# Kernel optimization log

Measured on AMD Instinct MI355X. Metric: run time of the kernel, lower is better.

Reference implementation:

```python
import jax, jax.numpy as jnp
import numpy as np

B, N, T, E = 8, 512, 2048, 4096
D, TD, L = 768, 128, 4
V, TYPES = 30522, 64
MAX_NODE_LEN = 512


def setup_inputs() -> dict:
    key = jax.random.key(0)
    ks = jax.random.split(key, 12)
    tok_per_node = T // N  # 4 tokens per node
    node_types = jax.random.randint(ks[0], (B, N), 0, TYPES)
    node_token_ids = jax.random.randint(ks[1], (B, T), 0, V)
    token_seg_ids = jnp.tile(jnp.arange(T, dtype=jnp.int32) // tok_per_node, (B, 1))
    node_token_lens = jnp.full((B, N), tok_per_node, dtype=jnp.int32)
    graph_node_lens = jnp.full((B,), N, dtype=jnp.int32)
    edge_src = jax.random.randint(ks[2], (B, E), 0, N)
    edge_dst = jax.random.randint(ks[3], (B, E), 0, N)
    # edges_attrs used as PyG edge_weight (original passes LongTensor); cast to float
    edge_weight = jax.random.randint(ks[4], (B, E), 1, 4).astype(jnp.float32)
    s = 0.02
    type_table = jax.random.normal(ks[5], (TYPES, TD)) * s
    word_emb = jax.random.normal(ks[6], (V, D)) * s
    fusion_w = jax.random.normal(ks[7], (TD + D, D)) * s
    fusion_b = jnp.zeros((D,), jnp.float32)
    ggnn_w = jax.random.normal(ks[8], (L, D, D)) * s  # per-layer message weight
    gru_w_ih = jax.random.normal(ks[9], (3 * D, D)) * s  # [W_ir; W_iz; W_in]
    gru_w_hh = jax.random.normal(ks[10], (3 * D, D)) * s
    gru_b_ih = jnp.zeros((3 * D,), jnp.float32)
    gru_b_hh = jnp.zeros((3 * D,), jnp.float32)
    return dict(node_types=node_types, node_token_ids=node_token_ids,
                token_seg_ids=token_seg_ids, node_token_lens=node_token_lens,
                graph_node_lens=graph_node_lens, edge_src=edge_src,
                edge_dst=edge_dst, edge_weight=edge_weight,
                type_table=type_table, word_emb=word_emb,
                fusion_w=fusion_w, fusion_b=fusion_b, ggnn_w=ggnn_w,
                gru_w_ih=gru_w_ih, gru_w_hh=gru_w_hh,
                gru_b_ih=gru_b_ih, gru_b_hh=gru_b_hh)


def reference(node_types, node_token_ids, token_seg_ids, node_token_lens,
              graph_node_lens, edge_src, edge_dst, edge_weight,
              type_table, word_emb, fusion_w, fusion_b, ggnn_w,
              gru_w_ih, gru_w_hh, gru_b_ih, gru_b_hh):
    # --- embed lookups ---
    type_e = type_table[node_types]          # [B, N, TD]
    tok_e = word_emb[node_token_ids]         # [B, T, D]
    # --- ragged per-node token segment-mean ---
    seg_sum = jax.vmap(lambda d, s: jax.ops.segment_sum(d, s, num_segments=N))(
        tok_e, token_seg_ids)                # [B, N, D]
    text_e = seg_sum / node_token_lens[..., None].astype(seg_sum.dtype)
    # --- embed fusion ---
    fused = jnp.concatenate([type_e, text_e], axis=-1)  # [B, N, TD+D]
    h = jnp.einsum('bnf,fd->bnd', fused, fusion_w) + fusion_b  # [B, N, D]

    # --- GatedGraphConv: L rounds of (linear -> weighted scatter-add -> GRU) ---
    def scatter(m, src, dst, w):
        return jnp.zeros((N, m.shape[-1]), m.dtype).at[dst].add(m[src] * w[:, None])

    for l in range(L):
        m = jnp.einsum('bnd,de->bne', h, ggnn_w[l])
        agg = jax.vmap(scatter)(m, edge_src, edge_dst, edge_weight)  # [B, N, D]
        gi = agg @ gru_w_ih.T + gru_b_ih
        gh = h @ gru_w_hh.T + gru_b_hh
        ir, iz, in_ = jnp.split(gi, 3, axis=-1)
        hr, hz, hn = jnp.split(gh, 3, axis=-1)
        r = jax.nn.sigmoid(ir + hr)
        z = jax.nn.sigmoid(iz + hz)
        n = jnp.tanh(in_ + r * hn)
        h = (1.0 - z) * n + z * h

    # --- copy first min(node_lens, max_node_len) rows into zero-initialized res ---
    W = min(N, MAX_NODE_LEN)
    keep = jnp.minimum(graph_node_lens, MAX_NODE_LEN)           # [B]
    valid = jnp.arange(W)[None, :] < keep[:, None]              # [B, W]
    return jnp.where(valid[..., None], h[:, :W], 0.0)           # [B, W, D]
```

## Files before the change

kernel.cpp:

```cpp
#include <hip/hip_runtime.h>
#include <hip/hip_bf16.h>
#include <math.h>

namespace {
constexpr int B_  = 8;
constexpr int N_  = 512;
constexpr int T_  = 2048;
constexpr int E_  = 4096;
constexpr int D_  = 768;
constexpr int TD_ = 128;
constexpr int L_  = 4;
constexpr int F_  = TD_ + D_;
constexpr int G3_ = 3 * D_;
constexpr int BN  = B_ * N_;
constexpr int W_  = 512;
constexpr int TPN = T_ / N_;
}

typedef short bf16x8 __attribute__((ext_vector_type(8)));
typedef float f32x4  __attribute__((ext_vector_type(4)));

typedef const __attribute__((address_space(1))) void* gas1_cvp;
typedef __attribute__((address_space(3))) void*       as3_vp;

__device__ __forceinline__ unsigned short f2b(float f) {
    union { float f; unsigned u; } v; v.f = f;
    unsigned r = v.u + 0x7FFFu + ((v.u >> 16) & 1u);
    return (unsigned short)(r >> 16);
}
__device__ __forceinline__ float b2f(unsigned short u) {
    union { unsigned u; float f; } v; v.u = ((unsigned)u) << 16;
    return v.f;
}


__global__ void embed_fuse_kernel(const int* __restrict__ node_types,
                                  const int* __restrict__ tok_ids,
                                  const int* __restrict__ lens,
                                  const float* __restrict__ type_table,
                                  const float* __restrict__ word_emb,
                                  unsigned short* __restrict__ fused_bf)
{
    int i = blockIdx.x * blockDim.x + threadIdx.x;
    if (i >= BN * (F_ / 4)) return;
    int c4 = i % (F_ / 4);
    int bn = i / (F_ / 4);
    if (c4 < TD_ / 4) {
        int ty = node_types[bn];
        float4 v = *(const float4*)&type_table[(long long)ty * TD_ + c4 * 4];
        *(ushort4*)&fused_bf[(long long)bn * F_ + c4 * 4] =
            make_ushort4(f2b(v.x), f2b(v.y), f2b(v.z), f2b(v.w));
    } else {
        int d4 = c4 - TD_ / 4;
        int b  = bn / N_;
        int nn = bn % N_;
        float inv = 1.0f / (float)lens[bn];
        const int* tp = &tok_ids[b * T_ + nn * TPN];
        float sx = 0.f, sy = 0.f, sz = 0.f, sw = 0.f;
#pragma unroll
        for (int j = 0; j < TPN; ++j) {
            int tok = tp[j];
            float4 e = *(const float4*)&word_emb[(long long)tok * D_ + d4 * 4];
            sx += e.x; sy += e.y; sz += e.z; sw += e.w;
        }
        *(ushort4*)&fused_bf[(long long)bn * F_ + TD_ + d4 * 4] =
            make_ushort4(f2b(sx * inv), f2b(sy * inv), f2b(sz * inv), f2b(sw * inv));
    }
}

__global__ void adj_build_kernel(const int* __restrict__ esrc,
                                 const int* __restrict__ edst,
                                 const float* __restrict__ ew,
                                 float* __restrict__ adj)
{
    int i = blockIdx.x * blockDim.x + threadIdx.x;
    if (i >= B_ * E_) return;
    int b = i / E_;
    int s = esrc[i];
    int d = edst[i];
    atomicAdd(&adj[((long long)b * N_ + d) * N_ + s], ew[i]);
}


__global__ void cvt_f32_bf16(const float* __restrict__ s, unsigned short* __restrict__ d, int n4)
{
    int i = blockIdx.x * blockDim.x + threadIdx.x;
    if (i >= n4) return;
    float4 v = ((const float4*)s)[i];
    ((ushort4*)d)[i] = make_ushort4(f2b(v.x), f2b(v.y), f2b(v.z), f2b(v.w));
}

__global__ void transpose_cvt(const float* __restrict__ s, unsigned short* __restrict__ d,
                              int R, int C)
{
    __shared__ float t[32][33];
    long long lo = (long long)blockIdx.z * R * C;
    s += lo; d += lo;
    int c0 = blockIdx.x * 32, r0 = blockIdx.y * 32;
    int tx = threadIdx.x, ty = threadIdx.y;
#pragma unroll
    for (int j = 0; j < 4; ++j)
        t[ty + j * 8][tx] = s[(long long)(r0 + ty + j * 8) * C + c0 + tx];
    __syncthreads();
#pragma unroll
    for (int j = 0; j < 4; ++j)
        d[(long long)(c0 + ty + j * 8) * R + r0 + tx] = f2b(t[tx][ty + j * 8]);
}


template <int MODE>
__global__ __launch_bounds__(256)
void gemm_mfma(const unsigned short* __restrict__ Ag,
               const unsigned short* __restrict__ Bg,
               void* __restrict__ Cg, void* __restrict__ C2g,
               const float* __restrict__ bias,
               int M, int N, int K, long long sA, long long sB, long long sC)
{
    __shared__ __align__(16) short As[128 * 32];
    __shared__ __align__(16) short Bs[128 * 32];

    const int tid  = threadIdx.x;
    const int lane = tid & 63;
    const int wv   = tid >> 6;
    const int wr   = wv >> 1, wc = wv & 1;
    const int row0 = blockIdx.y * 128;
    const int col0 = blockIdx.x * 128;

    const unsigned short* A  = Ag + blockIdx.z * sA;
    const unsigned short* Bm = Bg + blockIdx.z * sB;

    f32x4 acc[4][4] = {};

    const int srow = lane >> 2;
    const int sk   = (lane & 3) * 8;

    const int fr = lane & 15;
    const int kc = (lane >> 4) * 8;

    for (int k0 = 0; k0 < K; k0 += 32) {
#pragma unroll
        for (int r = 0; r < 2; ++r) {
            const unsigned short* ga = A  + (long long)(row0 + r * 64 + wv * 16 + srow) * K + k0 + sk;
            __builtin_amdgcn_global_load_lds((gas1_cvp)ga,
                (as3_vp)(As + (r * 64 + wv * 16) * 32), 16, 0, 0);
            const unsigned short* gb = Bm + (long long)(col0 + r * 64 + wv * 16 + srow) * K + k0 + sk;
            __builtin_amdgcn_global_load_lds((gas1_cvp)gb,
                (as3_vp)(Bs + (r * 64 + wv * 16) * 32), 16, 0, 0);
        }
        __syncthreads();

        bf16x8 fa[4], fb[4];
#pragma unroll
        for (int m = 0; m < 4; ++m)
            fa[m] = *(const bf16x8*)&As[(wr * 64 + m * 16 + fr) * 32 + kc];
#pragma unroll
        for (int n = 0; n < 4; ++n)
            fb[n] = *(const bf16x8*)&Bs[(wc * 64 + n * 16 + fr) * 32 + kc];
#pragma unroll
        for (int m = 0; m < 4; ++m)
#pragma unroll
            for (int n = 0; n < 4; ++n)
                acc[m][n] = __builtin_amdgcn_mfma_f32_16x16x32_bf16(fa[m], fb[n], acc[m][n], 0, 0, 0);
        __syncthreads();
    }

    const int fq = lane >> 4;
#pragma unroll
    for (int m = 0; m < 4; ++m) {
        const int gr = row0 + wr * 64 + m * 16 + fq * 4;
#pragma unroll
        for (int n = 0; n < 4; ++n) {
            const int gc = col0 + wc * 64 + n * 16 + fr;
            float v0 = acc[m][n][0], v1 = acc[m][n][1], v2 = acc[m][n][2], v3 = acc[m][n][3];
            if (bias != nullptr) {
                float bv = bias[gc];
                v0 += bv; v1 += bv; v2 += bv; v3 += bv;
            }
            if constexpr (MODE == 0 || MODE == 1) {
                float* C = (float*)Cg + blockIdx.z * sC;
                C[(long long)(gr + 0) * N + gc] = v0;
                C[(long long)(gr + 1) * N + gc] = v1;
                C[(long long)(gr + 2) * N + gc] = v2;
                C[(long long)(gr + 3) * N + gc] = v3;
                if constexpr (MODE == 1) {
                    unsigned short* C2 = (unsigned short*)C2g;
                    C2[(long long)(gr + 0) * N + gc] = f2b(v0);
                    C2[(long long)(gr + 1) * N + gc] = f2b(v1);
                    C2[(long long)(gr + 2) * N + gc] = f2b(v2);
                    C2[(long long)(gr + 3) * N + gc] = f2b(v3);
                }
            } else if constexpr (MODE == 2) {
                unsigned short* C = (unsigned short*)Cg + blockIdx.z * sC;
                C[(long long)(gr + 0) * N + gc] = f2b(v0);
                C[(long long)(gr + 1) * N + gc] = f2b(v1);
                C[(long long)(gr + 2) * N + gc] = f2b(v2);
                C[(long long)(gr + 3) * N + gc] = f2b(v3);
            } else {
                unsigned short* C = (unsigned short*)Cg;
                int b = gr >> 9;
                int s = gr & 511;
                ushort4 pk = make_ushort4(f2b(v0), f2b(v1), f2b(v2), f2b(v3));
                *(ushort4*)&C[((long long)b * N + gc) * 512 + s] = pk;
            }
        }
    }
}


__global__ void gru_kernel(const unsigned short* __restrict__ gi,
                           const unsigned short* __restrict__ gh,
                           const float* __restrict__ bih, const float* __restrict__ bhh,
                           float* __restrict__ h, unsigned short* __restrict__ hb)
{
    int i = blockIdx.x * blockDim.x + threadIdx.x;
    if (i >= BN * (D_ / 4)) return;
    int d4 = i % (D_ / 4);
    int rn = i / (D_ / 4);
    int d = d4 * 4;
    const unsigned short* gir = gi + (long long)rn * G3_;
    const unsigned short* ghr = gh + (long long)rn * G3_;
    ushort4 uir = *(const ushort4*)&gir[d];
    ushort4 uiz = *(const ushort4*)&gir[D_ + d];
    ushort4 uin = *(const ushort4*)&gir[2 * D_ + d];
    ushort4 uhr = *(const ushort4*)&ghr[d];
    ushort4 uhz = *(const ushort4*)&ghr[D_ + d];
    ushort4 uhn = *(const ushort4*)&ghr[2 * D_ + d];
    float4 hv = *(const float4*)&h[(long long)rn * D_ + d];

    float a_ir[4] = {b2f(uir.x), b2f(uir.y), b2f(uir.z), b2f(uir.w)};
    float a_iz[4] = {b2f(uiz.x), b2f(uiz.y), b2f(uiz.z), b2f(uiz.w)};
    float a_in[4] = {b2f(uin.x), b2f(uin.y), b2f(uin.z), b2f(uin.w)};
    float a_hr[4] = {b2f(uhr.x), b2f(uhr.y), b2f(uhr.z), b2f(uhr.w)};
    float a_hz[4] = {b2f(uhz.x), b2f(uhz.y), b2f(uhz.z), b2f(uhz.w)};
    float a_hn[4] = {b2f(uhn.x), b2f(uhn.y), b2f(uhn.z), b2f(uhn.w)};
    float a_h[4]  = {hv.x, hv.y, hv.z, hv.w};
    float outv[4];
#pragma unroll
    for (int u = 0; u < 4; ++u) {
        float r = 1.f / (1.f + expf(-(a_ir[u] + bih[d + u] + a_hr[u] + bhh[d + u])));
        float z = 1.f / (1.f + expf(-(a_iz[u] + bih[D_ + d + u] + a_hz[u] + bhh[D_ + d + u])));
        float n = tanhf(a_in[u] + bih[2 * D_ + d + u] + r * (a_hn[u] + bhh[2 * D_ + d + u]));
        outv[u] = (1.f - z) * n + z * a_h[u];
    }
    float4 o; o.x = outv[0]; o.y = outv[1]; o.z = outv[2]; o.w = outv[3];
    *(float4*)&h[(long long)rn * D_ + d] = o;
    *(ushort4*)&hb[(long long)rn * D_ + d] = make_ushort4(f2b(outv[0]), f2b(outv[1]),
                                                          f2b(outv[2]), f2b(outv[3]));
}


__global__ void out_mask_kernel(const int* __restrict__ gl, float* __restrict__ h)
{
    int i = blockIdx.x * blockDim.x + threadIdx.x;
    if (i >= B_ * W_ * (D_ / 4)) return;
    int d4 = i % (D_ / 4);
    int bw = i / (D_ / 4);
    int b = bw / W_;
    int w = bw % W_;
    int keep = min(gl[b], W_);
    if (w >= keep)
        *(float4*)&h[((long long)b * W_ + w) * D_ + d4 * 4] = make_float4(0.f, 0.f, 0.f, 0.f);
}


extern "C" void kernel_launch(void* const* d_in, const int* in_sizes, int n_in,
                              void* d_out, int out_size, void* d_ws, size_t ws_size,
                              hipStream_t stream)
{
    (void)in_sizes; (void)n_in; (void)out_size; (void)ws_size;

    const int*   node_types      = (const int*)d_in[0];
    const int*   node_token_ids  = (const int*)d_in[1];
    const int*   node_token_lens = (const int*)d_in[3];
    const int*   graph_node_lens = (const int*)d_in[4];
    const int*   edge_src        = (const int*)d_in[5];
    const int*   edge_dst        = (const int*)d_in[6];
    const float* edge_weight     = (const float*)d_in[7];
    const float* type_table      = (const float*)d_in[8];
    const float* word_emb        = (const float*)d_in[9];
    const float* fusion_w        = (const float*)d_in[10];
    const float* fusion_b        = (const float*)d_in[11];
    const float* ggnn_w          = (const float*)d_in[12];
    const float* gru_w_ih        = (const float*)d_in[13];
    const float* gru_w_hh        = (const float*)d_in[14];
    const float* gru_b_ih        = (const float*)d_in[15];
    const float* gru_b_hh        = (const float*)d_in[16];

    float* h = (float*)d_out;

    char* p = (char*)d_ws;
    auto carve = [&](size_t bytes) { char* r = p; p += (bytes + 255) & ~(size_t)255; return r; };

    unsigned short* gi_bf   = (unsigned short*)carve((size_t)BN * G3_ * 2);
    unsigned short* gh_bf   = (unsigned short*)carve((size_t)BN * G3_ * 2);
    unsigned short* h_bf    = (unsigned short*)carve((size_t)BN * D_ * 2);
    unsigned short* fused_bf= (unsigned short*)carve((size_t)BN * F_ * 2);
    float*          adj     = (float*)carve((size_t)B_ * N_ * N_ * 4);
    unsigned short* adj_bf  = (unsigned short*)carve((size_t)B_ * N_ * N_ * 2);
    unsigned short* mT      = (unsigned short*)carve((size_t)B_ * D_ * N_ * 2);
    unsigned short* agg_bf  = (unsigned short*)carve((size_t)BN * D_ * 2);
    unsigned short* fwT     = (unsigned short*)carve((size_t)D_ * F_ * 2);
    unsigned short* gwT     = (unsigned short*)carve((size_t)L_ * D_ * D_ * 2);
    unsigned short* wih_bf  = (unsigned short*)carve((size_t)G3_ * D_ * 2);
    unsigned short* whh_bf  = (unsigned short*)carve((size_t)G3_ * D_ * 2);

    hipMemsetAsync(adj, 0, (size_t)B_ * N_ * N_ * 4, stream);

    {   int n = BN * (F_ / 4);
        embed_fuse_kernel<<<(n + 255) / 256, 256, 0, stream>>>(
            node_types, node_token_ids, node_token_lens, type_table, word_emb, fused_bf); }
    {   int n = B_ * E_;
        adj_build_kernel<<<(n + 255) / 256, 256, 0, stream>>>(edge_src, edge_dst, edge_weight, adj); }

    cvt_f32_bf16<<<(B_ * N_ * N_ / 4 + 255) / 256, 256, 0, stream>>>(adj, adj_bf, B_ * N_ * N_ / 4);
    cvt_f32_bf16<<<(G3_ * D_ / 4 + 255) / 256, 256, 0, stream>>>(gru_w_ih, wih_bf, G3_ * D_ / 4);
    cvt_f32_bf16<<<(G3_ * D_ / 4 + 255) / 256, 256, 0, stream>>>(gru_w_hh, whh_bf, G3_ * D_ / 4);
    transpose_cvt<<<dim3(D_ / 32, F_ / 32, 1), dim3(32, 8), 0, stream>>>(fusion_w, fwT, F_, D_);
    transpose_cvt<<<dim3(D_ / 32, D_ / 32, L_), dim3(32, 8), 0, stream>>>(ggnn_w, gwT, D_, D_);

    dim3 blk(256);
    gemm_mfma<1><<<dim3(D_ / 128, BN / 128, 1), blk, 0, stream>>>(
        fused_bf, fwT, h, h_bf, fusion_b, BN, D_, F_, 0, 0, 0);

    for (int l = 0; l < L_; ++l) {
        gemm_mfma<3><<<dim3(D_ / 128, BN / 128, 1), blk, 0, stream>>>(
            h_bf, gwT + (size_t)l * D_ * D_, mT, nullptr, nullptr, BN, D_, D_, 0, 0, 0);
        gemm_mfma<2><<<dim3(D_ / 128, N_ / 128, B_), blk, 0, stream>>>(
            adj_bf, mT, agg_bf, nullptr, nullptr, N_, D_, N_,
            (long long)N_ * N_, (long long)D_ * N_, (long long)N_ * D_);
        gemm_mfma<2><<<dim3(G3_ / 128, BN / 128, 1), blk, 0, stream>>>(
            agg_bf, wih_bf, gi_bf, nullptr, nullptr, BN, G3_, D_, 0, 0, 0);
        gemm_mfma<2><<<dim3(G3_ / 128, BN / 128, 1), blk, 0, stream>>>(
            h_bf, whh_bf, gh_bf, nullptr, nullptr, BN, G3_, D_, 0, 0, 0);
        int n = BN * (D_ / 4);
        gru_kernel<<<(n + 255) / 256, 256, 0, stream>>>(gi_bf, gh_bf, gru_b_ih, gru_b_hh, h, h_bf);
    }

    {   int n = B_ * W_ * (D_ / 4);
        out_mask_kernel<<<(n + 255) / 256, 256, 0, stream>>>(graph_node_lens, h); }
}
```

Measured before the change: 723.9 us.

## Double-buffer GEMM LDS, merge GRU GEMMs, fuse mask and weight conversions

The GEMM main loop now uses two LDS buffers so the next K-tile's global-to-LDS load is issued before computing on the current one, aiming to hide load latency. The two GRU input and hidden GEMMs are merged into one launch with a z dimension of 2. The two weight bf16 conversions are combined into a single kernel, and the output masking moves into the final GRU step. These cut launch count and improve GEMM overlap, but double the LDS per block, which may lower occupancy.

```diff
diff --git a/kernel.cpp b/kernel.cpp
--- a/kernel.cpp
+++ b/kernel.cpp
@@ -90,6 +90,21 @@
     ((ushort4*)d)[i] = make_ushort4(f2b(v.x), f2b(v.y), f2b(v.z), f2b(v.w));
 }
 
+__global__ void cvt2_f32_bf16(const float* __restrict__ s0, unsigned short* __restrict__ d0,
+                              const float* __restrict__ s1, unsigned short* __restrict__ d1,
+                              int n4each)
+{
+    int i = blockIdx.x * blockDim.x + threadIdx.x;
+    if (i < n4each) {
+        float4 v = ((const float4*)s0)[i];
+        ((ushort4*)d0)[i] = make_ushort4(f2b(v.x), f2b(v.y), f2b(v.z), f2b(v.w));
+    } else if (i < 2 * n4each) {
+        int j = i - n4each;
+        float4 v = ((const float4*)s1)[j];
+        ((ushort4*)d1)[j] = make_ushort4(f2b(v.x), f2b(v.y), f2b(v.z), f2b(v.w));
+    }
+}
+
 __global__ void transpose_cvt(const float* __restrict__ s, unsigned short* __restrict__ d,
                               int R, int C)
 {
@@ -109,16 +124,12 @@
 
 
 template <int MODE>
-__global__ __launch_bounds__(256)
-void gemm_mfma(const unsigned short* __restrict__ Ag,
-               const unsigned short* __restrict__ Bg,
-               void* __restrict__ Cg, void* __restrict__ C2g,
-               const float* __restrict__ bias,
-               int M, int N, int K, long long sA, long long sB, long long sC)
-{
-    __shared__ __align__(16) short As[128 * 32];
-    __shared__ __align__(16) short Bs[128 * 32];
-
+__device__ __forceinline__ void gemm_body(
+    const unsigned short* __restrict__ A, const unsigned short* __restrict__ Bm,
+    void* __restrict__ Cg, void* __restrict__ C2g, const float* __restrict__ bias,
+    int M, int N, int K, long long zsC,
+    short* __restrict__ As0, short* __restrict__ Bs0)
+{
     const int tid  = threadIdx.x;
     const int lane = tid & 63;
     const int wv   = tid >> 6;
@@ -126,42 +137,50 @@
     const int row0 = blockIdx.y * 128;
     const int col0 = blockIdx.x * 128;
 
-    const unsigned short* A  = Ag + blockIdx.z * sA;
-    const unsigned short* Bm = Bg + blockIdx.z * sB;
-
     f32x4 acc[4][4] = {};
 
     const int srow = lane >> 2;
     const int sk   = (lane & 3) * 8;
-
-    const int fr = lane & 15;
-    const int kc = (lane >> 4) * 8;
-
-    for (int k0 = 0; k0 < K; k0 += 32) {
+    const int fr   = lane & 15;
+    const int kc   = (lane >> 4) * 8;
+
+    auto stage = [&](int buf, int k0) {
+        short* Ad = As0 + buf * (128 * 32);
+        short* Bd = Bs0 + buf * (128 * 32);
 #pragma unroll
         for (int r = 0; r < 2; ++r) {
-            const unsigned short* ga = A  + (long long)(row0 + r * 64 + wv * 16 + srow) * K + k0 + sk;
+            const unsigned short* ga = A + (long long)(row0 + r * 64 + wv * 16 + srow) * K + k0 + sk;
             __builtin_amdgcn_global_load_lds((gas1_cvp)ga,
-                (as3_vp)(As + (r * 64 + wv * 16) * 32), 16, 0, 0);
+                (as3_vp)(Ad + (r * 64 + wv * 16) * 32), 16, 0, 0);
             const unsigned short* gb = Bm + (long long)(col0 + r * 64 + wv * 16 + srow) * K + k0 + sk;
             __builtin_amdgcn_global_load_lds((gas1_cvp)gb,
-                (as3_vp)(Bs + (r * 64 + wv * 16) * 32), 16, 0, 0);
+                (as3_vp)(Bd + (r * 64 + wv * 16) * 32), 16, 0, 0);
         }
-        __syncthreads();
-
+    };
+
+    stage(0, 0);
+    __syncthreads();
+
+    const int nt = K >> 5;
+    int cur = 0;
+    for (int t = 0; t < nt; ++t) {
+        if (t + 1 < nt) stage(cur ^ 1, (t + 1) << 5);
+        const short* Ar = As0 + cur * (128 * 32);
+        const short* Br = Bs0 + cur * (128 * 32);
         bf16x8 fa[4], fb[4];
 #pragma unroll
         for (int m = 0; m < 4; ++m)
-            fa[m] = *(const bf16x8*)&As[(wr * 64 + m * 16 + fr) * 32 + kc];
+            fa[m] = *(const bf16x8*)&Ar[(wr * 64 + m * 16 + fr) * 32 + kc];
 #pragma unroll
         for (int n = 0; n < 4; ++n)
-            fb[n] = *(const bf16x8*)&Bs[(wc * 64 + n * 16 + fr) * 32 + kc];
+            fb[n] = *(const bf16x8*)&Br[(wc * 64 + n * 16 + fr) * 32 + kc];
 #pragma unroll
         for (int m = 0; m < 4; ++m)
 #pragma unroll
             for (int n = 0; n < 4; ++n)
                 acc[m][n] = __builtin_amdgcn_mfma_f32_16x16x32_bf16(fa[m], fb[n], acc[m][n], 0, 0, 0);
         __syncthreads();
+        cur ^= 1;
     }
 
     const int fq = lane >> 4;
@@ -177,7 +196,7 @@
                 v0 += bv; v1 += bv; v2 += bv; v3 += bv;
             }
             if constexpr (MODE == 0 || MODE == 1) {
-                float* C = (float*)Cg + blockIdx.z * sC;
+                float* C = (float*)Cg + zsC;
                 C[(long long)(gr + 0) * N + gc] = v0;
                 C[(long long)(gr + 1) * N + gc] = v1;
                 C[(long long)(gr + 2) * N + gc] = v2;
@@ -190,7 +209,7 @@
                     C2[(long long)(gr + 3) * N + gc] = f2b(v3);
                 }
             } else if constexpr (MODE == 2) {
-                unsigned short* C = (unsigned short*)Cg + blockIdx.z * sC;
+                unsigned short* C = (unsigned short*)Cg + zsC;
                 C[(long long)(gr + 0) * N + gc] = f2b(v0);
                 C[(long long)(gr + 1) * N + gc] = f2b(v1);
                 C[(long long)(gr + 2) * N + gc] = f2b(v2);
@@ -206,11 +225,43 @@
     }
 }
 
+template <int MODE>
+__global__ __launch_bounds__(256)
+void gemm_mfma(const unsigned short* __restrict__ Ag,
+               const unsigned short* __restrict__ Bg,
+               void* __restrict__ Cg, void* __restrict__ C2g,
+               const float* __restrict__ bias,
+               int M, int N, int K, long long sA, long long sB, long long sC)
+{
+    __shared__ __align__(16) short As[2 * 128 * 32];
+    __shared__ __align__(16) short Bs[2 * 128 * 32];
+    gemm_body<MODE>(Ag + blockIdx.z * sA, Bg + blockIdx.z * sB, Cg, C2g, bias,
+                    M, N, K, blockIdx.z * sC, As, Bs);
+}
+
+template <int MODE>
+__global__ __launch_bounds__(256)
+void gemm_mfma_dual(const unsigned short* __restrict__ A0,
+                    const unsigned short* __restrict__ A1,
+                    const unsigned short* __restrict__ B0,
+                    const unsigned short* __restrict__ B1,
+                    void* __restrict__ C0, void* __restrict__ C1,
+                    int M, int N, int K)
+{
+    __shared__ __align__(16) short As[2 * 128 * 32];
+    __shared__ __align__(16) short Bs[2 * 128 * 32];
+    const unsigned short* A  = blockIdx.z ? A1 : A0;
+    const unsigned short* Bm = blockIdx.z ? B1 : B0;
+    void* C = blockIdx.z ? C1 : C0;
+    gemm_body<MODE>(A, Bm, C, nullptr, nullptr, M, N, K, 0, As, Bs);
+}
+
 
 __global__ void gru_kernel(const unsigned short* __restrict__ gi,
                            const unsigned short* __restrict__ gh,
                            const float* __restrict__ bih, const float* __restrict__ bhh,
-                           float* __restrict__ h, unsigned short* __restrict__ hb)
+                           float* __restrict__ h, unsigned short* __restrict__ hb,
+                           const int* __restrict__ gl)
 {
     int i = blockIdx.x * blockDim.x + threadIdx.x;
     if (i >= BN * (D_ / 4)) return;
@@ -242,24 +293,15 @@
         float n = tanhf(a_in[u] + bih[2 * D_ + d + u] + r * (a_hn[u] + bhh[2 * D_ + d + u]));
         outv[u] = (1.f - z) * n + z * a_h[u];
     }
+    if (gl != nullptr) {
+        int b = rn / N_;
+        int w = rn % N_;
+        if (w >= min(gl[b], W_)) { outv[0] = outv[1] = outv[2] = outv[3] = 0.f; }
+    }
     float4 o; o.x = outv[0]; o.y = outv[1]; o.z = outv[2]; o.w = outv[3];
     *(float4*)&h[(long long)rn * D_ + d] = o;
     *(ushort4*)&hb[(long long)rn * D_ + d] = make_ushort4(f2b(outv[0]), f2b(outv[1]),
                                                           f2b(outv[2]), f2b(outv[3]));
-}
-
-
-__global__ void out_mask_kernel(const int* __restrict__ gl, float* __restrict__ h)
-{
-    int i = blockIdx.x * blockDim.x + threadIdx.x;
-    if (i >= B_ * W_ * (D_ / 4)) return;
-    int d4 = i % (D_ / 4);
-    int bw = i / (D_ / 4);
-    int b = bw / W_;
-    int w = bw % W_;
-    int keep = min(gl[b], W_);
-    if (w >= keep)
-        *(float4*)&h[((long long)b * W_ + w) * D_ + d4 * 4] = make_float4(0.f, 0.f, 0.f, 0.f);
 }
 
 
@@ -312,9 +354,9 @@
     {   int n = B_ * E_;
         adj_build_kernel<<<(n + 255) / 256, 256, 0, stream>>>(edge_src, edge_dst, edge_weight, adj); }
 
+    cvt2_f32_bf16<<<(2 * G3_ * D_ / 4 + 255) / 256, 256, 0, stream>>>(
+        gru_w_ih, wih_bf, gru_w_hh, whh_bf, G3_ * D_ / 4);
     cvt_f32_bf16<<<(B_ * N_ * N_ / 4 + 255) / 256, 256, 0, stream>>>(adj, adj_bf, B_ * N_ * N_ / 4);
-    cvt_f32_bf16<<<(G3_ * D_ / 4 + 255) / 256, 256, 0, stream>>>(gru_w_ih, wih_bf, G3_ * D_ / 4);
-    cvt_f32_bf16<<<(G3_ * D_ / 4 + 255) / 256, 256, 0, stream>>>(gru_w_hh, whh_bf, G3_ * D_ / 4);
     transpose_cvt<<<dim3(D_ / 32, F_ / 32, 1), dim3(32, 8), 0, stream>>>(fusion_w, fwT, F_, D_);
     transpose_cvt<<<dim3(D_ / 32, D_ / 32, L_), dim3(32, 8), 0, stream>>>(ggnn_w, gwT, D_, D_);
 
@@ -328,14 +370,11 @@
         gemm_mfma<2><<<dim3(D_ / 128, N_ / 128, B_), blk, 0, stream>>>(
             adj_bf, mT, agg_bf, nullptr, nullptr, N_, D_, N_,
             (long long)N_ * N_, (long long)D_ * N_, (long long)N_ * D_);
-        gemm_mfma<2><<<dim3(G3_ / 128, BN / 128, 1), blk, 0, stream>>>(
-            agg_bf, wih_bf, gi_bf, nullptr, nullptr, BN, G3_, D_, 0, 0, 0);
-        gemm_mfma<2><<<dim3(G3_ / 128, BN / 128, 1), blk, 0, stream>>>(
-            h_bf, whh_bf, gh_bf, nullptr, nullptr, BN, G3_, D_, 0, 0, 0);
+        gemm_mfma_dual<2><<<dim3(G3_ / 128, BN / 128, 2), blk, 0, stream>>>(
+            agg_bf, h_bf, wih_bf, whh_bf, gi_bf, gh_bf, BN, G3_, D_);
         int n = BN * (D_ / 4);
-        gru_kernel<<<(n + 255) / 256, 256, 0, stream>>>(gi_bf, gh_bf, gru_b_ih, gru_b_hh, h, h_bf);
-    }
-
-    {   int n = B_ * W_ * (D_ / 4);
-        out_mask_kernel<<<(n + 255) / 256, 256, 0, stream>>>(graph_node_lens, h); }
-}
+        gru_kernel<<<(n + 255) / 256, 256, 0, stream>>>(
+            gi_bf, gh_bf, gru_b_ih, gru_b_hh, h, h_bf,
+            (l == L_ - 1) ? graph_node_lens : nullptr);
+    }
+}
```

Measured after the change: 642.2 us. 11.3% less time.
